# Optimization experiments

Measured on AMD Instinct MI355X. Metric: run time of the kernel, lower is better.

The kernel has to match this reference:

```python
import jax, jax.numpy as jnp
import numpy as np
import math

V, D, L, H, T, B = 32000, 1024, 4, 16, 2048, 1
HD = D // H
EPS = 1e-5

def _pos_encoding(T, D):
    pos = jnp.arange(T, dtype=jnp.float32)[:, None]                      # [T,1]
    div = jnp.exp(jnp.arange(0, D, 2, dtype=jnp.float32) * (-math.log(10000.0) / D))
    ang = pos * div                                                      # [T,D/2]
    pe = jnp.zeros((T, D), dtype=jnp.float32)
    pe = pe.at[:, 0::2].set(jnp.sin(ang)).at[:, 1::2].set(jnp.cos(ang))
    return pe

def _layernorm(x, g, b):
    mu = jnp.mean(x, axis=-1, keepdims=True)
    var = jnp.mean(jnp.square(x - mu), axis=-1, keepdims=True)
    return (x - mu) * jax.lax.rsqrt(var + EPS) * g + b

def setup_inputs() -> dict:
    key = jax.random.key(0)
    ks = jax.random.split(key, 16)
    s = 0.02
    inp = {
        'idx': jax.random.randint(ks[0], (B, T), 0, V),
        'embed': jax.random.normal(ks[1], (V, D), jnp.float32) * s,
        'Wq': jax.random.normal(ks[2], (L, D, D), jnp.float32) * s,
        'Wk': jax.random.normal(ks[3], (L, D, D), jnp.float32) * s,
        'Wv': jax.random.normal(ks[4], (L, D, D), jnp.float32) * s,
        'Wo': jax.random.normal(ks[5], (L, D, D), jnp.float32) * s,
        'bq': jnp.zeros((L, D), jnp.float32),
        'bk': jnp.zeros((L, D), jnp.float32),
        'bv': jnp.zeros((L, D), jnp.float32),
        'bo': jnp.zeros((L, D), jnp.float32),
        'ln1_g': jnp.ones((L, D), jnp.float32), 'ln1_b': jnp.zeros((L, D), jnp.float32),
        'ln2_g': jnp.ones((L, D), jnp.float32), 'ln2_b': jnp.zeros((L, D), jnp.float32),
        'w1': jax.random.normal(ks[6], (L, D, 4 * D), jnp.float32) * s,
        'b1': jnp.zeros((L, 4 * D), jnp.float32),
        'w2': jax.random.normal(ks[7], (L, 4 * D, D), jnp.float32) * s,
        'b2': jnp.zeros((L, D), jnp.float32),
        'lnf_g': jnp.ones((D,), jnp.float32), 'lnf_b': jnp.zeros((D,), jnp.float32),
        'head_w': jax.random.normal(ks[8], (D, V), jnp.float32) * s,
    }
    return inp

def _forward(idx, embed, Wq, Wk, Wv, Wo, bq, bk, bv, bo,
             ln1_g, ln1_b, ln2_g, ln2_b, w1, b1, w2, b2, lnf_g, lnf_b, head_w):
    Bs, Ts = idx.shape
    x = embed[idx] + _pos_encoding(Ts, embed.shape[1])[None]            # [B,T,D]
    causal = jnp.tril(jnp.ones((Ts, Ts), dtype=bool))                   # [T,T]
    scale = 1.0 / math.sqrt(HD)

    def block(x, p):
        wq, wk, wv, wo, q_b, k_b, v_b, o_b, g1, be1, g2, be2, fw1, fb1, fw2, fb2 = p
        h = _layernorm(x, g1, be1)
        q = (h @ wq + q_b).reshape(Bs, Ts, H, HD)
        k = (h @ wk + k_b).reshape(Bs, Ts, H, HD)
        v = (h @ wv + v_b).reshape(Bs, Ts, H, HD)
        att = jnp.einsum('bthd,bshd->bhts', q, k) * scale               # [B,H,T,T]
        att = jnp.where(causal, att, -jnp.inf)
        att = jax.nn.softmax(att, axis=-1)
        o = jnp.einsum('bhts,bshd->bthd', att, v).reshape(Bs, Ts, -1)
        x = x + (o @ wo + o_b)
        h2 = _layernorm(x, g2, be2)
        ff = jax.nn.gelu(h2 @ fw1 + fb1, approximate=False) @ fw2 + fb2
        x = x + ff
        return x, None

    params = (Wq, Wk, Wv, Wo, bq, bk, bv, bo, ln1_g, ln1_b, ln2_g, ln2_b, w1, b1, w2, b2)
    x, _ = jax.lax.scan(block, x, params)
    x = _layernorm(x, lnf_g, lnf_b)
    return x @ head_w                                                   # [B,T,V]

def reference(idx, embed, Wq, Wk, Wv, Wo, bq, bk, bv, bo,
              ln1_g, ln1_b, ln2_g, ln2_b, w1, b1, w2, b2, lnf_g, lnf_b, head_w):
    return _forward(idx, embed, Wq, Wk, Wv, Wo, bq, bk, bv, bo,
                    ln1_g, ln1_b, ln2_g, ln2_b, w1, b1, w2, b2, lnf_g, lnf_b, head_w)
```

## Files before the change

kernel.cpp:

```cpp
#include <hip/hip_runtime.h>
#include <cstdint>

using u16 = unsigned short;
using u32 = unsigned int;
typedef __bf16  bf16x8 __attribute__((ext_vector_type(8)));
typedef float   f32x4  __attribute__((ext_vector_type(4)));
typedef float   f32x16 __attribute__((ext_vector_type(16)));

__device__ __forceinline__ u16 f2b(float x) {
    u32 u = __builtin_bit_cast(u32, x);
    u = (u + 0x7fffu + ((u >> 16) & 1u)) >> 16;
    return (u16)u;
}

__device__ __forceinline__ f32x4 mfma16(bf16x8 a, bf16x8 b, f32x4 c) {
    return __builtin_amdgcn_mfma_f32_16x16x32_bf16(a, b, c, 0, 0, 0);
}
__device__ __forceinline__ f32x16 mfma32(bf16x8 a, bf16x8 b, f32x16 c) {
    return __builtin_amdgcn_mfma_f32_32x32x16_bf16(a, b, c, 0, 0, 0);
}

__device__ __forceinline__ void gload16(const void* g, void* lds) {
    auto gp = (__attribute__((address_space(1))) void*)(uintptr_t)g;
    auto lp = (__attribute__((address_space(3))) void*)(uintptr_t)lds;
    __builtin_amdgcn_global_load_lds(gp, lp, 16, 0, 0);
}

__device__ __forceinline__ int2 swz_bmbn(int nbm) {
    const int nwg = gridDim.x, orig = blockIdx.x;
    const int q = nwg >> 3, r = nwg & 7;
    const int xcd = orig & 7, lin = orig >> 3;
    const int id = (xcd < r ? xcd * (q + 1) : r * (q + 1) + (xcd - r) * q) + lin;
    return make_int2(id % nbm, id / nbm);
}

template <int BM, int KC, int EPI>
__global__ __launch_bounds__(BM == 256 ? 512 : 256, 2) void gemm_deep_k(
    const u16* __restrict__ A, int lda, const u16* __restrict__ Bt, int ldb,
    const float* __restrict__ bias, float* __restrict__ outf,
    u16* __restrict__ outb, int N, int nbm, int sk, long long sOut,
    u16* __restrict__ out2)
{
    constexpr int WCOLS = (BM == 256) ? 4 : 2;
    constexpr int MF    = BM / 32;
    constexpr int NF    = 4;
    constexpr int SLOT  = BM * 32;
    constexpr int HALF  = (BM / 2) * 32;
    constexpr int H     = KC >> 5;
    constexpr int RPG   = (MF + NF) / 4;
    constexpr int MPG   = (MF * NF) / 4;

    __shared__ __align__(16) u16 lsA[4][SLOT];
    __shared__ __align__(16) u16 lsB[4][SLOT];

    const int s = blockIdx.y;
    A  += (size_t)s * sk;
    Bt += (size_t)s * sk;
    if (EPI == 4) outf += (size_t)s * sOut;

    const int2 bb = swz_bmbn(nbm);
    const int m0 = bb.x * BM, n0 = bb.y * BM;
    const int tid = threadIdx.x;
    const int w = tid >> 6, lane = tid & 63;
    const int wr = (w / WCOLS) * (MF * 16), wc = (w % WCOLS) * 64;
    const int lr = lane & 15, lg = lane >> 4;
    const int rsw = (lg ^ ((lr >> 1) & 3)) * 8;

    const int trow = tid >> 2;
    const int ksw8 = ((tid & 3) ^ ((tid >> 3) & 3)) * 8;
    const u16* aA = A  + (size_t)(m0 + trow) * lda + ksw8;
    const u16* aB = Bt + (size_t)(n0 + trow) * ldb + ksw8;
    u16* dA = &lsA[0][0] + trow * 32 + (tid & 3) * 8;
    u16* dB = &lsB[0][0] + trow * 32 + (tid & 3) * 8;

    f32x4 acc[MF][NF] = {};

    auto stage = [&](int h) {
        const int sl = h & 3;
        const int koff = h * 32;
        gload16(aA + koff,                          dA + sl * SLOT);
        gload16(aA + koff + (size_t)(BM / 2) * lda, dA + sl * SLOT + HALF);
        gload16(aB + koff,                          dB + sl * SLOT);
        gload16(aB + koff + (size_t)(BM / 2) * ldb, dB + sl * SLOT + HALF);
    };

    bf16x8 ra0[MF], rb0[NF], ra1[MF], rb1[NF];
    auto lreadAll = [&](bf16x8* af, bf16x8* bf, int h) {
        const int sl = h & 3;
#pragma unroll
        for (int m = 0; m < MF; m++)
            af[m] = *(const bf16x8*)&lsA[sl][(wr + m * 16 + lr) * 32 + rsw];
#pragma unroll
        for (int n = 0; n < NF; n++)
            bf[n] = *(const bf16x8*)&lsB[sl][(wc + n * 16 + lr) * 32 + rsw];
    };

    auto body = [&](int h, bf16x8* aC, bf16x8* bC, bf16x8* aN, bf16x8* bN) {
        if (h + 3 < H) stage(h + 3);
        __builtin_amdgcn_sched_barrier(0);
        asm volatile("s_waitcnt lgkmcnt(0)" ::: "memory");
        const int rem = H - 1 - h;
        if (rem >= 3)      asm volatile("s_waitcnt vmcnt(8)" ::: "memory");
        else if (rem == 2) asm volatile("s_waitcnt vmcnt(4)" ::: "memory");
        else if (rem == 1) asm volatile("s_waitcnt vmcnt(0)" ::: "memory");
        __builtin_amdgcn_s_barrier();
        __builtin_amdgcn_sched_barrier(0);
        const int sl1 = (h + 1) & 3;
        const bool doRead = (h + 1 < H);
#pragma unroll
        for (int g = 0; g < 4; ++g) {
            if (doRead) {
#pragma unroll
                for (int t = g * RPG; t < (g + 1) * RPG; ++t) {
                    if (t < MF) aN[t]      = *(const bf16x8*)&lsA[sl1][(wr + t * 16 + lr) * 32 + rsw];
                    else        bN[t - MF] = *(const bf16x8*)&lsB[sl1][(wc + (t - MF) * 16 + lr) * 32 + rsw];
                }
            }
            __builtin_amdgcn_sched_barrier(0);
            __builtin_amdgcn_s_setprio(1);
#pragma unroll
            for (int i = g * MPG; i < (g + 1) * MPG; ++i)
                acc[i / NF][i % NF] = mfma16(aC[i / NF], bC[i % NF], acc[i / NF][i % NF]);
            __builtin_amdgcn_s_setprio(0);
            __builtin_amdgcn_sched_barrier(0);
        }
    };

    stage(0); stage(1); stage(2);
    asm volatile("s_waitcnt vmcnt(8)" ::: "memory");
    __builtin_amdgcn_s_barrier();
    lreadAll(ra0, rb0, 0);

#pragma unroll
    for (int h = 0; h < H; h += 2) {
        body(h,     ra0, rb0, ra1, rb1);
        body(h + 1, ra1, rb1, ra0, rb0);
    }

#pragma unroll
    for (int n = 0; n < NF; n++) {
        const int gc = n0 + wc + n * 16 + lr;
        float bv = 0.f;
        if constexpr (EPI == 0 || EPI == 1 || EPI == 5) bv = bias[gc];
#pragma unroll
        for (int m = 0; m < MF; m++) {
            const int grb = m0 + wr + m * 16 + lg * 4;
#pragma unroll
            for (int r = 0; r < 4; r++) {
                float v = acc[m][n][r] + bv;
                if constexpr (EPI == 1) v = 0.5f * v * (1.f + erff(v * 0.70710678118654752f));
                const size_t o = (size_t)(grb + r) * N + gc;
                if constexpr (EPI == 3)      __builtin_nontemporal_store(v, &outf[o]);
                else if constexpr (EPI == 4) outf[o] = v;
                else {
                    const u16 bvv = f2b(v);
                    outb[o] = bvv;
                    if constexpr (EPI == 5) {
                        if (gc >= 2048)
                            out2[(size_t)(gc - 2048) * 2048 + grb + r] = bvv;
                    }
                }
            }
        }
    }
}

__global__ __launch_bounds__(256) void reduce_ln_k(
    const float* __restrict__ pbuf, int S,
    const float* __restrict__ bias,
    float* __restrict__ x,
    const float* __restrict__ g, const float* __restrict__ bln,
    u16* __restrict__ hb)
{
    __shared__ float red[8];
    const int row = blockIdx.x, tid = threadIdx.x;
    const int w = tid >> 6, lane = tid & 63;
    const size_t base = (size_t)row * 256 + tid;
    float4 v = ((const float4*)x)[base];
    for (int s = 0; s < S; ++s) {
        const float4 p = ((const float4*)pbuf)[(size_t)s * 524288 + base];
        v.x += p.x; v.y += p.y; v.z += p.z; v.w += p.w;
    }
    const float4 bb = ((const float4*)bias)[tid];
    v.x += bb.x; v.y += bb.y; v.z += bb.z; v.w += bb.w;
    ((float4*)x)[base] = v;

    float s1 = v.x + v.y + v.z + v.w;
#pragma unroll
    for (int d = 1; d < 64; d <<= 1) s1 += __shfl_xor(s1, d);
    if (lane == 0) red[w] = s1;
    __syncthreads();
    const float mu = (red[0] + red[1] + red[2] + red[3]) * (1.f / 1024.f);
    const float d0 = v.x - mu, d1 = v.y - mu, d2 = v.z - mu, d3 = v.w - mu;
    float s2 = d0 * d0 + d1 * d1 + d2 * d2 + d3 * d3;
#pragma unroll
    for (int d = 1; d < 64; d <<= 1) s2 += __shfl_xor(s2, d);
    if (lane == 0) red[4 + w] = s2;
    __syncthreads();
    const float var = (red[4] + red[5] + red[6] + red[7]) * (1.f / 1024.f);
    const float rs = rsqrtf(var + 1e-5f);
    const float4 gv = ((const float4*)g)[tid];
    const float4 bv = ((const float4*)bln)[tid];
    u32 p0 = (u32)f2b(d0 * rs * gv.x + bv.x) | ((u32)f2b(d1 * rs * gv.y + bv.y) << 16);
    u32 p1 = (u32)f2b(d2 * rs * gv.z + bv.z) | ((u32)f2b(d3 * rs * gv.w + bv.w) << 16);
    ((uint2*)(hb + (size_t)row * 1024))[tid] = make_uint2(p0, p1);
}

__global__ __launch_bounds__(256) void flash_attn_k(
    const u16* __restrict__ qkv, const u16* __restrict__ vT, u16* __restrict__ out)
{
    constexpr int DS = 3072, T = 2048;
    __shared__ float mrg[2][64][32];
    __shared__ float msh[2][32], lsh[2][32];
    __shared__ u16   sbuf[2][32 * 68];
    const int w = threadIdx.x >> 6, lane = threadIdx.x & 63;
    const int lq = lane & 31, hi = lane >> 5;
    const int hoff = blockIdx.y * 64;
    const int pair = w >> 1, par = w & 1;
    const int qt = (pair == 0) ? blockIdx.x : 63 - blockIdx.x;
    const int q0 = qt * 32;
    const int qg = q0 + lq;

    const u16* qp = qkv + (size_t)qg * DS + hoff;
    const u16* kp = qkv + 1024 + hoff;

    bf16x8 qf[4];
#pragma unroll
    for (int d = 0; d < 4; d++)
        qf[d] = *(const bf16x8*)(qp + d * 16 + hi * 8);

    f32x16 o0 = {}, o1 = {};
    float m_r = -1e30f, l_r = 0.f;

    const int ntiles = (qt >> 1) + 1;
    for (int t = par; t < ntiles; t += 2) {
        const int kv0 = t * 64;
        f32x16 s0 = {}, s1 = {};
        {
            const u16* kb0 = kp + (size_t)(kv0 + lq) * DS + hi * 8;
            const u16* kb1 = kb0 + (size_t)32 * DS;
#pragma unroll
            for (int d = 0; d < 4; d++) {
                s0 = mfma32(*(const bf16x8*)(kb0 + d * 16), qf[d], s0);
                s1 = mfma32(*(const bf16x8*)(kb1 + d * 16), qf[d], s1);
            }
        }
        float p[32];
        float mx = -1e30f;
#pragma unroll
        for (int r = 0; r < 16; r++) {
            const int kvl = (r & 3) + 8 * (r >> 2) + 4 * hi;
            float v0 = (kv0 + kvl      <= qg) ? s0[r] * 0.125f : -1e30f;
            float v1 = (kv0 + 32 + kvl <= qg) ? s1[r] * 0.125f : -1e30f;
            p[r] = v0; p[16 + r] = v1;
            mx = fmaxf(mx, fmaxf(v0, v1));
        }
        mx = fmaxf(mx, __shfl_xor(mx, 32));
        const float mn = fmaxf(m_r, mx);
        const float alpha = __expf(m_r - mn);
        m_r = mn;
        float ls = 0.f;
#pragma unroll
        for (int i = 0; i < 32; i++) { p[i] = __expf(p[i] - mn); ls += p[i]; }
        ls += __shfl_xor(ls, 32);
        l_r = l_r * alpha + ls;
#pragma unroll
        for (int r = 0; r < 16; r++) { o0[r] *= alpha; o1[r] *= alpha; }
#pragma unroll
        for (int sub = 0; sub < 2; sub++) {
            u32 pw[8], x[8];
#pragma unroll
            for (int i = 0; i < 8; i++)
                pw[i] = (u32)f2b(p[sub * 16 + 2 * i]) | ((u32)f2b(p[sub * 16 + 2 * i + 1]) << 16);
#pragma unroll
            for (int i = 0; i < 8; i++) x[i] = __shfl_xor(pw[i], 32);
            u32 b0[4], b1[4];
            b0[0] = hi ? x[2]  : pw[0];  b0[1] = hi ? x[3]  : pw[1];
            b0[2] = hi ? pw[2] : x[0];   b0[3] = hi ? pw[3] : x[1];
            b1[0] = hi ? x[6]  : pw[4];  b1[1] = hi ? x[7]  : pw[5];
            b1[2] = hi ? pw[6] : x[4];   b1[3] = hi ? pw[7] : x[5];
            bf16x8 B0 = __builtin_bit_cast(bf16x8, *(const uint4*)b0);
            bf16x8 B1 = __builtin_bit_cast(bf16x8, *(const uint4*)b1);
            const u16* vb = vT + (size_t)(hoff + lq) * T + kv0 + sub * 32 + hi * 8;
            o0 = mfma32(*(const bf16x8*)vb, B0, o0);
            o0 = mfma32(*(const bf16x8*)(vb + 16), B1, o0);
            const u16* vb1 = vb + (size_t)32 * T;
            o1 = mfma32(*(const bf16x8*)vb1, B0, o1);
            o1 = mfma32(*(const bf16x8*)(vb1 + 16), B1, o1);
        }
    }

    __syncthreads();
    if (par == 0) {
#pragma unroll
        for (int r = 0; r < 16; r++) {
            const int d = (r & 3) + 8 * (r >> 2) + 4 * hi;
            mrg[pair][d][lq]      = o0[r];
            mrg[pair][d + 32][lq] = o1[r];
        }
        if (hi == 0) { msh[pair][lq] = m_r; lsh[pair][lq] = l_r; }
    }
    __syncthreads();
    if (par == 1) {
        const float m0v = msh[pair][lq], l0v = lsh[pair][lq];
        const float M = fmaxf(m0v, m_r);
        const float f0 = __expf(m0v - M), f1 = __expf(m_r - M);
        const float linv = 1.f / (l0v * f0 + l_r * f1);
        u32* sb = (u32*)sbuf[pair];
#pragma unroll
        for (int r = 0; r < 16; r += 2) {
            const int d = (r & 3) + 8 * (r >> 2) + 4 * hi;
            float va = (mrg[pair][d][lq] * f0 + o0[r] * f1) * linv;
            float vb = (mrg[pair][d + 1][lq] * f0 + o0[r + 1] * f1) * linv;
            sb[lq * 34 + (d >> 1)] = (u32)f2b(va) | ((u32)f2b(vb) << 16);
            float vc = (mrg[pair][d + 32][lq] * f0 + o1[r] * f1) * linv;
            float vd = (mrg[pair][d + 33][lq] * f0 + o1[r + 1] * f1) * linv;
            sb[lq * 34 + ((d + 32) >> 1)] = (u32)f2b(vc) | ((u32)f2b(vd) << 16);
        }
#pragma unroll
        for (int ps = 0; ps < 8; ps++) {
            const int row = ps * 4 + (lane >> 4);
            const uint2 v = *(const uint2*)&sbuf[pair][row * 68 + (lane & 15) * 4];
            *(uint2*)(out + (size_t)(q0 + row) * 1024 + hoff + (lane & 15) * 4) = v;
        }
    }
}

__global__ __launch_bounds__(256) void transpose_cvt_k(
    const float* __restrict__ src, u16* __restrict__ dst, int K, int N,
    long long srcLS, long long dstLS)
{
    __shared__ float tf[32][132];
    src += (size_t)blockIdx.z * srcLS;
    dst += (size_t)blockIdx.z * dstLS;
    const int n0 = blockIdx.x * 128, k0 = blockIdx.y * 32;
    const int tid = threadIdx.x;
    const int tn = tid & 31, tk = tid >> 5;
#pragma unroll
    for (int p = 0; p < 4; ++p) {
        const int k = tk + p * 8;
        const float4 v = *(const float4*)&src[(size_t)(k0 + k) * N + n0 + tn * 4];
        *(float4*)&tf[k][tn * 4] = v;
    }
    __syncthreads();
    const int kq = (tid & 7) * 4;
    const int tn2 = tid >> 3;
#pragma unroll
    for (int w = 0; w < 4; ++w) {
        const int n = tn2 + w * 32;
        const u32 lo = (u32)f2b(tf[kq + 0][n]) | ((u32)f2b(tf[kq + 1][n]) << 16);
        const u32 hi = (u32)f2b(tf[kq + 2][n]) | ((u32)f2b(tf[kq + 3][n]) << 16);
        *(uint2*)&dst[(size_t)(n0 + n) * K + k0 + kq] = make_uint2(lo, hi);
    }
}

__global__ __launch_bounds__(256) void concat_bias_k(
    const float* __restrict__ bq, const float* __restrict__ bk,
    const float* __restrict__ bv, float* __restrict__ bcat)
{
    const int l = blockIdx.y;
    const int j = blockIdx.x * 256 + threadIdx.x;
    float v;
    if (j < 1024)      v = bq[l * 1024 + j];
    else if (j < 2048) v = bk[l * 1024 + j - 1024];
    else               v = bv[l * 1024 + j - 2048];
    bcat[l * 3072 + j] = v;
}

__global__ __launch_bounds__(256) void embed_pos_k(
    const int* __restrict__ idx, const float* __restrict__ emb, float* __restrict__ x)
{
    const int t = blockIdx.x, tid = threadIdx.x;
    const int tok = idx[t];
    float4 e = ((const float4*)(emb + (size_t)tok * 1024))[tid];
    const int d0 = tid * 4;
    const float c = -0.0089944730195080f;
    const float a0 = (float)t * expf((float)d0 * c);
    const float a1 = (float)t * expf((float)(d0 + 2) * c);
    e.x += sinf(a0); e.y += cosf(a0); e.z += sinf(a1); e.w += cosf(a1);
    ((float4*)(x + (size_t)t * 1024))[tid] = e;
}

__global__ __launch_bounds__(256) void layernorm_k(
    const float* __restrict__ x, const float* __restrict__ g,
    const float* __restrict__ b, u16* __restrict__ out)
{
    __shared__ float red[8];
    const int row = blockIdx.x, tid = threadIdx.x;
    const int w = tid >> 6, lane = tid & 63;
    const float4 v = ((const float4*)(x + (size_t)row * 1024))[tid];
    float s = v.x + v.y + v.z + v.w;
#pragma unroll
    for (int d = 1; d < 64; d <<= 1) s += __shfl_xor(s, d);
    if (lane == 0) red[w] = s;
    __syncthreads();
    const float mu = (red[0] + red[1] + red[2] + red[3]) * (1.f / 1024.f);
    const float d0 = v.x - mu, d1 = v.y - mu, d2 = v.z - mu, d3 = v.w - mu;
    float s2 = d0 * d0 + d1 * d1 + d2 * d2 + d3 * d3;
#pragma unroll
    for (int d = 1; d < 64; d <<= 1) s2 += __shfl_xor(s2, d);
    if (lane == 0) red[4 + w] = s2;
    __syncthreads();
    const float var = (red[4] + red[5] + red[6] + red[7]) * (1.f / 1024.f);
    const float rs = rsqrtf(var + 1e-5f);
    const float4 gv = ((const float4*)g)[tid];
    const float4 bv = ((const float4*)b)[tid];
    u32 p0 = (u32)f2b(d0 * rs * gv.x + bv.x) | ((u32)f2b(d1 * rs * gv.y + bv.y) << 16);
    u32 p1 = (u32)f2b(d2 * rs * gv.z + bv.z) | ((u32)f2b(d3 * rs * gv.w + bv.w) << 16);
    ((uint2*)(out + (size_t)row * 1024))[tid] = make_uint2(p0, p1);
}

extern "C" void kernel_launch(void* const* d_in, const int* in_sizes, int n_in,
                              void* d_out, int out_size, void* d_ws, size_t ws_size,
                              hipStream_t stream)
{
    const int*   idx   = (const int*)  d_in[0];
    const float* embed = (const float*)d_in[1];
    const float* Wq    = (const float*)d_in[2];
    const float* Wk    = (const float*)d_in[3];
    const float* Wv    = (const float*)d_in[4];
    const float* Wo    = (const float*)d_in[5];
    const float* bq    = (const float*)d_in[6];
    const float* bk    = (const float*)d_in[7];
    const float* bv    = (const float*)d_in[8];
    const float* bo    = (const float*)d_in[9];
    const float* ln1g  = (const float*)d_in[10];
    const float* ln1b  = (const float*)d_in[11];
    const float* ln2g  = (const float*)d_in[12];
    const float* ln2b  = (const float*)d_in[13];
    const float* w1    = (const float*)d_in[14];
    const float* b1    = (const float*)d_in[15];
    const float* w2    = (const float*)d_in[16];
    const float* b2    = (const float*)d_in[17];
    const float* lnfg  = (const float*)d_in[18];
    const float* lnfb  = (const float*)d_in[19];
    const float* headw = (const float*)d_in[20];

    char* ws = (char*)d_ws;
    auto alloc = [&](size_t bytes) {
        char* p = ws;
        ws += (bytes + 255) & ~(size_t)255;
        return p;
    };
    u16*   qkvT = (u16*)alloc((size_t)4 * 3072 * 1024 * 2);
    u16*   WoT  = (u16*)alloc((size_t)4 * 1024 * 1024 * 2);
    u16*   w1T  = (u16*)alloc((size_t)4 * 1024 * 4096 * 2);
    u16*   w2T  = (u16*)alloc((size_t)4 * 1024 * 4096 * 2);
    u16*   hT   = (u16*)alloc((size_t)32000 * 1024 * 2);
    float* bcat = (float*)alloc((size_t)4 * 3072 * 4);
    float* x    = (float*)alloc((size_t)2048 * 1024 * 4);
    u16*   hb   = (u16*)alloc((size_t)2048 * 1024 * 2);
    u16*   qkvb = (u16*)alloc((size_t)2048 * 3072 * 2);
    u16*   vTb  = (u16*)alloc((size_t)2048 * 1024 * 2);
    u16*   ab   = (u16*)alloc((size_t)2048 * 1024 * 2);
    u16*   ff   = (u16*)alloc((size_t)2048 * 4096 * 2);
    float* pbuf = (float*)d_out;

    transpose_cvt_k<<<dim3(8, 32, 4),   256, 0, stream>>>(Wq, qkvT,            1024, 1024, 1048576, 3145728);
    transpose_cvt_k<<<dim3(8, 32, 4),   256, 0, stream>>>(Wk, qkvT + 1048576,  1024, 1024, 1048576, 3145728);
    transpose_cvt_k<<<dim3(8, 32, 4),   256, 0, stream>>>(Wv, qkvT + 2097152,  1024, 1024, 1048576, 3145728);
    transpose_cvt_k<<<dim3(8, 32, 4),   256, 0, stream>>>(Wo, WoT,             1024, 1024, 1048576, 1048576);
    transpose_cvt_k<<<dim3(32, 32, 4),  256, 0, stream>>>(w1, w1T,             1024, 4096, 4194304, 4194304);
    transpose_cvt_k<<<dim3(8, 128, 4),  256, 0, stream>>>(w2, w2T,             4096, 1024, 4194304, 4194304);
    transpose_cvt_k<<<dim3(250, 32, 1), 256, 0, stream>>>(headw, hT,           1024, 32000, 0, 0);
    concat_bias_k<<<dim3(12, 4), 256, 0, stream>>>(bq, bk, bv, bcat);

    embed_pos_k<<<dim3(2048), 256, 0, stream>>>(idx, embed, x);
    layernorm_k<<<dim3(2048), 256, 0, stream>>>(x, ln1g, ln1b, hb);

    for (int l = 0; l < 4; ++l) {
        gemm_deep_k<128, 1024, 5><<<dim3(384), 256, 0, stream>>>(
            hb, 1024, qkvT + (size_t)l * 3145728, 1024,
            bcat + l * 3072, nullptr, qkvb, 3072, 16, 0, 0, vTb);
        flash_attn_k<<<dim3(32, 16), 256, 0, stream>>>(qkvb, vTb, ab);
        gemm_deep_k<128, 512, 4><<<dim3(128, 2), 256, 0, stream>>>(
            ab, 1024, WoT + (size_t)l * 1048576, 1024,
            nullptr, pbuf, nullptr, 1024, 16, 512, 2097152, nullptr);
        reduce_ln_k<<<dim3(2048), 256, 0, stream>>>(pbuf, 2, bo + l * 1024, x,
                                                    ln2g + l * 1024, ln2b + l * 1024, hb);
        gemm_deep_k<128, 1024, 1><<<dim3(512), 256, 0, stream>>>(
            hb, 1024, w1T + (size_t)l * 4194304, 1024,
            b1 + l * 4096, nullptr, ff, 4096, 16, 0, 0, nullptr);
        gemm_deep_k<128, 1024, 4><<<dim3(128, 4), 256, 0, stream>>>(
            ff, 4096, w2T + (size_t)l * 4194304, 4096,
            nullptr, pbuf, nullptr, 1024, 16, 1024, 2097152, nullptr);
        const float* ng = (l < 3) ? (ln1g + (l + 1) * 1024) : lnfg;
        const float* nb = (l < 3) ? (ln1b + (l + 1) * 1024) : lnfb;
        reduce_ln_k<<<dim3(2048), 256, 0, stream>>>(pbuf, 4, b2 + l * 1024, x, ng, nb, hb);
    }
    gemm_deep_k<256, 1024, 3><<<dim3(1000), 512, 0, stream>>>(
        hb, 1024, hT, 1024, nullptr, (float*)d_out, nullptr, 32000, 8, 0, 0, nullptr);
}
```

Before: 1.014 ms.

## Add dedicated head GEMM with split LDS reads; move V transpose to separate kernel

```diff
diff --git a/kernel.cpp b/kernel.cpp
--- a/kernel.cpp
+++ b/kernel.cpp
@@ -34,21 +34,129 @@
     return make_int2(id % nbm, id / nbm);
 }
 
-template <int BM, int KC, int EPI>
-__global__ __launch_bounds__(BM == 256 ? 512 : 256, 2) void gemm_deep_k(
+__global__ __launch_bounds__(512, 2) void gemm_head_k(
+    const u16* __restrict__ A, const u16* __restrict__ Bt,
+    float* __restrict__ out, int M, int N)
+{
+    constexpr int KV = 1024;
+    constexpr int H  = KV >> 5;
+    __shared__ __align__(16) u16 lsA[4][256 * 32];
+    __shared__ __align__(16) u16 lsB[4][256 * 32];
+    const int nbm = M >> 8;
+    const int2 bb = swz_bmbn(nbm);
+    const int m0 = bb.x * 256, n0 = bb.y * 256;
+    const int tid = threadIdx.x;
+    const int w = tid >> 6, lane = tid & 63;
+    const int wr = (w >> 2) * 128, wc = (w & 3) * 64;
+    const int lr = lane & 15, lg = lane >> 4;
+    const int rsw = (lg ^ ((lr >> 1) & 3)) * 8;
+
+    const int trow = tid >> 2;
+    const int ksw8 = ((tid & 3) ^ ((tid >> 3) & 3)) * 8;
+    const u16* aA = A  + (size_t)(m0 + trow) * KV + ksw8;
+    const u16* aB = Bt + (size_t)(n0 + trow) * KV + ksw8;
+    u16* dA = &lsA[0][0] + trow * 32 + (tid & 3) * 8;
+    u16* dB = &lsB[0][0] + trow * 32 + (tid & 3) * 8;
+
+    f32x4 acc[8][4] = {};
+
+    auto stage = [&](int h) {
+        const int sl = h & 3;
+        const int ko = h * 32;
+        gload16(aA + ko,                      dA + sl * 8192);
+        gload16(aA + ko + (size_t)128 * KV,   dA + sl * 8192 + 4096);
+        gload16(aB + ko,                      dB + sl * 8192);
+        gload16(aB + ko + (size_t)128 * KV,   dB + sl * 8192 + 4096);
+    };
+
+    bf16x8 ra0[8], rb0[4], ra1[8], rb1[4];
+    auto rdLow = [&](bf16x8* ra, bf16x8* rb, int h) {
+        const int sl = h & 3;
+#pragma unroll
+        for (int m = 0; m < 4; m++)
+            ra[m] = *(const bf16x8*)&lsA[sl][(wr + m * 16 + lr) * 32 + rsw];
+#pragma unroll
+        for (int n = 0; n < 4; n++)
+            rb[n] = *(const bf16x8*)&lsB[sl][(wc + n * 16 + lr) * 32 + rsw];
+    };
+    auto rdHigh = [&](bf16x8* ra, int h) {
+        const int sl = h & 3;
+#pragma unroll
+        for (int m = 4; m < 8; m++)
+            ra[m] = *(const bf16x8*)&lsA[sl][(wr + m * 16 + lr) * 32 + rsw];
+    };
+
+    auto body = [&](int h, bf16x8* raC, bf16x8* rbC, bf16x8* raN, bf16x8* rbN) {
+        rdHigh(raC, h);
+        if (h + 3 < H) stage(h + 3);
+        const int rem = H - 1 - h;
+        if (rem >= 3)      asm volatile("s_waitcnt vmcnt(8)" ::: "memory");
+        else if (rem == 2) asm volatile("s_waitcnt vmcnt(4)" ::: "memory");
+        else if (rem == 1) asm volatile("s_waitcnt vmcnt(0)" ::: "memory");
+        __builtin_amdgcn_s_barrier();
+        asm volatile("s_waitcnt lgkmcnt(4)" ::: "memory");
+        __builtin_amdgcn_sched_barrier(0);
+        __builtin_amdgcn_s_setprio(1);
+#pragma unroll
+        for (int m = 0; m < 4; m++)
+#pragma unroll
+            for (int n = 0; n < 4; n++)
+                acc[m][n] = mfma16(raC[m], rbC[n], acc[m][n]);
+        __builtin_amdgcn_s_setprio(0);
+        __builtin_amdgcn_sched_barrier(0);
+        __builtin_amdgcn_s_barrier();
+        if (h + 1 < H) rdLow(raN, rbN, h + 1);
+        __builtin_amdgcn_sched_barrier(0);
+        __builtin_amdgcn_s_barrier();
+        if (h + 1 < H) asm volatile("s_waitcnt lgkmcnt(8)" ::: "memory");
+        else           asm volatile("s_waitcnt lgkmcnt(0)" ::: "memory");
+        __builtin_amdgcn_sched_barrier(0);
+        __builtin_amdgcn_s_setprio(1);
+#pragma unroll
+        for (int m = 4; m < 8; m++)
+#pragma unroll
+            for (int n = 0; n < 4; n++)
+                acc[m][n] = mfma16(raC[m], rbC[n], acc[m][n]);
+        __builtin_amdgcn_s_setprio(0);
+        __builtin_amdgcn_sched_barrier(0);
+        __builtin_amdgcn_s_barrier();
+    };
+
+    stage(0); stage(1); stage(2);
+    asm volatile("s_waitcnt vmcnt(8)" ::: "memory");
+    __builtin_amdgcn_s_barrier();
+    rdLow(ra0, rb0, 0);
+
+#pragma unroll
+    for (int h = 0; h < H; h += 2) {
+        body(h,     ra0, rb0, ra1, rb1);
+        body(h + 1, ra1, rb1, ra0, rb0);
+    }
+
+#pragma unroll
+    for (int m = 0; m < 8; m++) {
+        const int gr = m0 + wr + m * 16 + lg * 4;
+#pragma unroll
+        for (int r = 0; r < 4; r++) {
+            float* orow = out + (size_t)(gr + r) * N + n0 + wc + lr;
+#pragma unroll
+            for (int n = 0; n < 4; n++)
+                orow[n * 16] = acc[m][n][r];
+        }
+    }
+}
+
+template <int KC, int EPI>
+__global__ __launch_bounds__(256, 2) void gemm_deep_k(
     const u16* __restrict__ A, int lda, const u16* __restrict__ Bt, int ldb,
     const float* __restrict__ bias, float* __restrict__ outf,
-    u16* __restrict__ outb, int N, int nbm, int sk, long long sOut,
-    u16* __restrict__ out2)
-{
-    constexpr int WCOLS = (BM == 256) ? 4 : 2;
-    constexpr int MF    = BM / 32;
-    constexpr int NF    = 4;
-    constexpr int SLOT  = BM * 32;
-    constexpr int HALF  = (BM / 2) * 32;
-    constexpr int H     = KC >> 5;
-    constexpr int RPG   = (MF + NF) / 4;
-    constexpr int MPG   = (MF * NF) / 4;
+    u16* __restrict__ outb, int N, int nbm, int sk, long long sOut)
+{
+    constexpr int MF   = 4;
+    constexpr int NF   = 4;
+    constexpr int SLOT = 128 * 32;
+    constexpr int HALF = 64 * 32;
+    constexpr int H    = KC >> 5;
 
     __shared__ __align__(16) u16 lsA[4][SLOT];
     __shared__ __align__(16) u16 lsB[4][SLOT];
@@ -59,10 +167,10 @@
     if (EPI == 4) outf += (size_t)s * sOut;
 
     const int2 bb = swz_bmbn(nbm);
-    const int m0 = bb.x * BM, n0 = bb.y * BM;
+    const int m0 = bb.x * 128, n0 = bb.y * 128;
     const int tid = threadIdx.x;
     const int w = tid >> 6, lane = tid & 63;
-    const int wr = (w / WCOLS) * (MF * 16), wc = (w % WCOLS) * 64;
+    const int wr = (w >> 1) * 64, wc = (w & 1) * 64;
     const int lr = lane & 15, lg = lane >> 4;
     const int rsw = (lg ^ ((lr >> 1) & 3)) * 8;
 
@@ -78,10 +186,10 @@
     auto stage = [&](int h) {
         const int sl = h & 3;
         const int koff = h * 32;
-        gload16(aA + koff,                          dA + sl * SLOT);
-        gload16(aA + koff + (size_t)(BM / 2) * lda, dA + sl * SLOT + HALF);
-        gload16(aB + koff,                          dB + sl * SLOT);
-        gload16(aB + koff + (size_t)(BM / 2) * ldb, dB + sl * SLOT + HALF);
+        gload16(aA + koff,                     dA + sl * SLOT);
+        gload16(aA + koff + (size_t)64 * lda,  dA + sl * SLOT + HALF);
+        gload16(aB + koff,                     dB + sl * SLOT);
+        gload16(aB + koff + (size_t)64 * ldb,  dB + sl * SLOT + HALF);
     };
 
     bf16x8 ra0[MF], rb0[NF], ra1[MF], rb1[NF];
@@ -111,7 +219,7 @@
         for (int g = 0; g < 4; ++g) {
             if (doRead) {
 #pragma unroll
-                for (int t = g * RPG; t < (g + 1) * RPG; ++t) {
+                for (int t = g * 2; t < g * 2 + 2; ++t) {
                     if (t < MF) aN[t]      = *(const bf16x8*)&lsA[sl1][(wr + t * 16 + lr) * 32 + rsw];
                     else        bN[t - MF] = *(const bf16x8*)&lsB[sl1][(wc + (t - MF) * 16 + lr) * 32 + rsw];
                 }
@@ -119,7 +227,7 @@
             __builtin_amdgcn_sched_barrier(0);
             __builtin_amdgcn_s_setprio(1);
 #pragma unroll
-            for (int i = g * MPG; i < (g + 1) * MPG; ++i)
+            for (int i = g * 4; i < g * 4 + 4; ++i)
                 acc[i / NF][i % NF] = mfma16(aC[i / NF], bC[i % NF], acc[i / NF][i % NF]);
             __builtin_amdgcn_s_setprio(0);
             __builtin_amdgcn_sched_barrier(0);
@@ -141,7 +249,7 @@
     for (int n = 0; n < NF; n++) {
         const int gc = n0 + wc + n * 16 + lr;
         float bv = 0.f;
-        if constexpr (EPI == 0 || EPI == 1 || EPI == 5) bv = bias[gc];
+        if constexpr (EPI == 0 || EPI == 1) bv = bias[gc];
 #pragma unroll
         for (int m = 0; m < MF; m++) {
             const int grb = m0 + wr + m * 16 + lg * 4;
@@ -150,16 +258,8 @@
                 float v = acc[m][n][r] + bv;
                 if constexpr (EPI == 1) v = 0.5f * v * (1.f + erff(v * 0.70710678118654752f));
                 const size_t o = (size_t)(grb + r) * N + gc;
-                if constexpr (EPI == 3)      __builtin_nontemporal_store(v, &outf[o]);
-                else if constexpr (EPI == 4) outf[o] = v;
-                else {
-                    const u16 bvv = f2b(v);
-                    outb[o] = bvv;
-                    if constexpr (EPI == 5) {
-                        if (gc >= 2048)
-                            out2[(size_t)(gc - 2048) * 2048 + grb + r] = bvv;
-                    }
-                }
+                if constexpr (EPI == 4) outf[o] = v;
+                else                    outb[o] = f2b(v);
             }
         }
     }
@@ -352,6 +452,21 @@
         const u32 hi = (u32)f2b(tf[kq + 2][n]) | ((u32)f2b(tf[kq + 3][n]) << 16);
         *(uint2*)&dst[(size_t)(n0 + n) * K + k0 + kq] = make_uint2(lo, hi);
     }
+}
+
+__global__ __launch_bounds__(256) void transpose_u16_k(
+    const u16* __restrict__ src, u16* __restrict__ dst, int R, int C, int srcStride)
+{
+    __shared__ u16 tile[32][33];
+    const int c0 = blockIdx.x * 32, r0 = blockIdx.y * 32;
+    const int tx = threadIdx.x & 31, ty = threadIdx.x >> 5;
+#pragma unroll
+    for (int r = 0; r < 32; r += 8)
+        tile[ty + r][tx] = src[(size_t)(r0 + ty + r) * srcStride + c0 + tx];
+    __syncthreads();
+#pragma unroll
+    for (int r = 0; r < 32; r += 8)
+        dst[(size_t)(c0 + ty + r) * R + r0 + tx] = tile[tx][ty + r];
 }
 
 __global__ __launch_bounds__(256) void concat_bias_k(
@@ -469,25 +584,25 @@
     layernorm_k<<<dim3(2048), 256, 0, stream>>>(x, ln1g, ln1b, hb);
 
     for (int l = 0; l < 4; ++l) {
-        gemm_deep_k<128, 1024, 5><<<dim3(384), 256, 0, stream>>>(
+        gemm_deep_k<1024, 0><<<dim3(384), 256, 0, stream>>>(
             hb, 1024, qkvT + (size_t)l * 3145728, 1024,
-            bcat + l * 3072, nullptr, qkvb, 3072, 16, 0, 0, vTb);
+            bcat + l * 3072, nullptr, qkvb, 3072, 16, 0, 0);
+        transpose_u16_k<<<dim3(32, 64), 256, 0, stream>>>(qkvb + 2048, vTb, 2048, 1024, 3072);
         flash_attn_k<<<dim3(32, 16), 256, 0, stream>>>(qkvb, vTb, ab);
-        gemm_deep_k<128, 512, 4><<<dim3(128, 2), 256, 0, stream>>>(
+        gemm_deep_k<512, 4><<<dim3(128, 2), 256, 0, stream>>>(
             ab, 1024, WoT + (size_t)l * 1048576, 1024,
-            nullptr, pbuf, nullptr, 1024, 16, 512, 2097152, nullptr);
+            nullptr, pbuf, nullptr, 1024, 16, 512, 2097152);
         reduce_ln_k<<<dim3(2048), 256, 0, stream>>>(pbuf, 2, bo + l * 1024, x,
                                                     ln2g + l * 1024, ln2b + l * 1024, hb);
-        gemm_deep_k<128, 1024, 1><<<dim3(512), 256, 0, stream>>>(
+        gemm_deep_k<1024, 1><<<dim3(512), 256, 0, stream>>>(
             hb, 1024, w1T + (size_t)l * 4194304, 1024,
-            b1 + l * 4096, nullptr, ff, 4096, 16, 0, 0, nullptr);
-        gemm_deep_k<128, 1024, 4><<<dim3(128, 4), 256, 0, stream>>>(
+            b1 + l * 4096, nullptr, ff, 4096, 16, 0, 0);
+        gemm_deep_k<1024, 4><<<dim3(128, 4), 256, 0, stream>>>(
             ff, 4096, w2T + (size_t)l * 4194304, 4096,
-            nullptr, pbuf, nullptr, 1024, 16, 1024, 2097152, nullptr);
+            nullptr, pbuf, nullptr, 1024, 16, 1024, 2097152);
         const float* ng = (l < 3) ? (ln1g + (l + 1) * 1024) : lnfg;
         const float* nb = (l < 3) ? (ln1b + (l + 1) * 1024) : lnfb;
         reduce_ln_k<<<dim3(2048), 256, 0, stream>>>(pbuf, 4, b2 + l * 1024, x, ng, nb, hb);
     }
-    gemm_deep_k<256, 1024, 3><<<dim3(1000), 512, 0, stream>>>(
-        hb, 1024, hT, 1024, nullptr, (float*)d_out, nullptr, 32000, 8, 0, 0, nullptr);
-}
+    gemm_head_k<<<dim3(1000), 512, 0, stream>>>(hb, hT, (float*)d_out, 2048, 32000);
+}
```

Measured after the change: 975.8 us. 1.04x faster.
